# Optimization experiments

Hardware: AMD Instinct MI355X
Metric: run time of the kernel (lower is better)

## Reference

```python
import jax, jax.numpy as jnp
import numpy as np

MIN_C = 1e-5   # base_c * DYNAMIC_CURVATURE_MIN_RATIO
MAX_C = 10.0   # base_c * DYNAMIC_CURVATURE_MAX_RATIO
T = 0.7
EPS = 1e-7
B, IN_DIM, HID, OUT_DIM = 4096, 4096, 4096, 1024


def _artanh(x):
    x = jnp.clip(x, -1.0 + 1e-5, 1.0 - 1e-5)
    return 0.5 * jnp.log1p(2.0 * x / (1.0 - x))


def _mobius_scalar_mul(r, x, c):
    # r: python float, x: [B,D], c: [B,1] per-row curvature
    sqrt_c = jnp.sqrt(c)
    norm = jnp.clip(jnp.linalg.norm(x, axis=-1, keepdims=True), EPS)
    arg = jnp.clip(sqrt_c * norm, EPS, 1.0 - 1e-5)
    return jnp.tanh(r * _artanh(arg)) * x / (sqrt_c * norm)


def _mobius_add(x, y, c):
    xy = jnp.sum(x * y, axis=-1, keepdims=True)
    x2 = jnp.sum(x * x, axis=-1, keepdims=True)
    y2 = jnp.sum(y * y, axis=-1, keepdims=True)
    num = (1.0 + 2.0 * c * xy + c * y2) * x + (1.0 - c * x2) * y
    den = 1.0 + 2.0 * c * xy + c * c * x2 * y2
    return num / jnp.clip(den, EPS)


def poincare_ball_layer(h, u, c, t):
    # geodesic-style layer: ((1-t) (*) h) (+) (t (*) u) on the Poincare ball
    return _mobius_add(_mobius_scalar_mul(1.0 - t, h, c),
                       _mobius_scalar_mul(t, u, c), c)


def setup_inputs() -> dict:
    key = jax.random.key(0)
    ks = jax.random.split(key, 8)
    std = 0.02  # WEIGHT_INIT_STD_IMPROVED
    return {
        "x": jax.random.normal(ks[0], (B, IN_DIM), jnp.float32),
        "W1": jax.random.normal(ks[1], (IN_DIM, HID), jnp.float32) * std,
        "b1": jnp.zeros((HID,), jnp.float32),
        "W2": jax.random.normal(ks[2], (HID, HID), jnp.float32) * std,
        "b2": jnp.zeros((HID,), jnp.float32),
        "Wout": jax.random.normal(ks[3], (HID, OUT_DIM), jnp.float32) * std,
        "bout": jnp.zeros((OUT_DIM,), jnp.float32),
        "curv_feat": jax.random.normal(ks[4], (16,), jnp.float32) * 0.01,
        "curv_scale": jnp.ones((1,), jnp.float32) * 0.1,
        "proj": jax.random.normal(ks[5], (IN_DIM, 16), jnp.float32),
    }


def reference(x, W1, b1, W2, b2, Wout, bout, curv_feat, curv_scale, proj):
    x_flat = x.reshape(x.shape[0], -1)
    h = jnp.tanh(x_flat @ W1 + b1)            # [B, HID]
    u = jax.nn.sigmoid(h @ W2 + b2)           # [B, HID]
    # adaptive curvature prediction (vectorized over batch)
    x_red = x_flat @ proj                     # [B, 16]
    feat_inter = x_red @ curv_feat            # [B]
    adj = jax.nn.sigmoid(feat_inter + curv_scale[0])
    c = MIN_C + (MAX_C - MIN_C) * adj         # [B]
    c = jnp.clip(c, MIN_C, MAX_C)[:, None]    # [B, 1]
    z = poincare_ball_layer(h, u, c, T)
    # NaN fallback per row (mirrors torch per-sample isnan check)
    z = jnp.where(jnp.any(jnp.isnan(z), axis=1, keepdims=True), h, z)
    return z @ Wout + bout
```

## Files before the change

kernel.cpp:

```cpp
#include <hip/hip_runtime.h>
#include <hip/hip_bf16.h>
#include <math.h>


typedef __attribute__((ext_vector_type(8))) __bf16 bf16x8;
typedef __attribute__((ext_vector_type(4))) float  f32x4;

constexpr int BATCH = 4096;
constexpr int IND   = 4096;
constexpr int HIDD  = 4096;
constexpr int OUTD  = 1024;
constexpr float T_C  = 0.7f;
constexpr float MINC = 1e-5f;
constexpr float MAXC = 10.0f;
constexpr float EPSV = 1e-7f;

__device__ __forceinline__ float bf2f(unsigned int us) {
    return __uint_as_float(us << 16);
}
__device__ __forceinline__ unsigned short f2bf(float f) {
    unsigned int u = __float_as_uint(f);
    u = (u + 0x7FFFu + ((u >> 16) & 1u)) >> 16;
    return (unsigned short)u;
}

__global__ __launch_bounds__(256)
void cast_curv(const float* __restrict__ x, const float* __restrict__ v,
               const float* __restrict__ cs,
               unsigned short* __restrict__ xb, float* __restrict__ c)
{
    const int row = blockIdx.x;
    const float* xr = x + (size_t)row * IND;
    unsigned short* ob = xb + (size_t)row * IND;
    float s = 0.f;
    for (int i = threadIdx.x; i < IND / 4; i += 256) {
        float4 w  = ((const float4*)xr)[i];
        float4 vv = ((const float4*)v)[i];
        s += w.x * vv.x + w.y * vv.y + w.z * vv.z + w.w * vv.w;
        ushort4 o;
        o.x = f2bf(w.x); o.y = f2bf(w.y); o.z = f2bf(w.z); o.w = f2bf(w.w);
        ((ushort4*)ob)[i] = o;
    }
    #pragma unroll
    for (int o = 32; o > 0; o >>= 1) s += __shfl_down(s, o, 64);
    __shared__ float red[4];
    if ((threadIdx.x & 63) == 0) red[threadIdx.x >> 6] = s;
    __syncthreads();
    if (threadIdx.x == 0) {
        float tot = red[0] + red[1] + red[2] + red[3];
        float adj = 1.0f / (1.0f + expf(-(tot + cs[0])));
        float cc  = MINC + (MAXC - MINC) * adj;
        c[row] = fminf(fmaxf(cc, MINC), MAXC);
    }
}

__global__ __launch_bounds__(256)
void transpose_cast(const float* __restrict__ in, unsigned short* __restrict__ out,
                    int K, int N)
{
    __shared__ float tile[32][33];
    const int k0 = blockIdx.y * 32;
    const int n0 = blockIdx.x * 32;
    const int t = threadIdx.x;
    #pragma unroll
    for (int i = 0; i < 4; i++) {
        int idx = t + i * 256;
        int r = idx >> 5, c = idx & 31;
        tile[r][c] = in[(size_t)(k0 + r) * N + n0 + c];
    }
    __syncthreads();
    #pragma unroll
    for (int i = 0; i < 4; i++) {
        int idx = t + i * 256;
        int r = idx >> 5, c = idx & 31;
        out[(size_t)(n0 + r) * K + k0 + c] = f2bf(tile[c][r]);
    }
}

template<int EPI>
__global__ __launch_bounds__(512)
void gemm256(const unsigned short* __restrict__ A,
             const unsigned short* __restrict__ Bt,
             const float* __restrict__ bias,
             unsigned short* __restrict__ outp,
             int N, int K)
{
    __shared__ unsigned short lds[4 * 256 * 64];
    unsigned short* Al = lds;
    unsigned short* Bl = lds + 2 * 256 * 64;

    const int t = threadIdx.x;
    const int w = t >> 6, l = t & 63;
    const int wr = w >> 2, wc = w & 3;
    const int lr = l & 15, lg = l >> 4;

    const int nwg = gridDim.x * gridDim.y;
    const int bid = blockIdx.y * gridDim.x + blockIdx.x;
    const int q8 = nwg >> 3, r8 = nwg & 7;
    const int xcd = bid & 7, off = bid >> 3;
    const int wgid = (xcd < r8 ? xcd * (q8 + 1) : r8 * (q8 + 1) + (xcd - r8) * q8) + off;
    const int by = wgid / gridDim.x;
    const int bx = wgid % gridDim.x;

    const int row0 = by * 256, col0 = bx * 256;
    const unsigned short* Ab = A  + (size_t)row0 * K;
    const unsigned short* Bb = Bt + (size_t)col0 * K;
    const int NT = K >> 6;

    f32x4 acc[8][4] = {};

    auto stage_half = [&](int kt, int buf, int mat, int h) {
        const int kb = kt * 128;
        const unsigned short* gb = mat ? Bb : Ab;
        unsigned short* lb = (mat ? Bl : Al) + buf * 16384 + h * 8192;
        #pragma unroll
        for (int qq = 0; qq < 2; qq++) {
            const int id  = qq * 512 + t;
            const int row = h * 128 + (id >> 3);
            const int cb  = (id & 7) * 16;
            const int scb = cb ^ ((row & 7) << 4);
            const char* src = (const char*)gb + (size_t)row * ((size_t)K * 2) + kb + scb;
            __builtin_amdgcn_global_load_lds(
                (const __attribute__((address_space(1))) unsigned int*)src,
                (__attribute__((address_space(3))) unsigned int*)(lb + id * 8), 16, 0, 0);
        }
    };

    stage_half(0, 0, 0, 0);
    stage_half(0, 0, 1, 0);
    stage_half(0, 0, 1, 1);
    stage_half(0, 0, 0, 1);
    asm volatile("s_waitcnt vmcnt(2)" ::: "memory");
    __builtin_amdgcn_s_barrier();

    const int sw = (lr & 7) << 4;
    const int c0 = (lg * 16) ^ sw;
    const int c1 = (64 + lg * 16) ^ sw;

    for (int kt = 0; kt < NT; ++kt) {
        const int buf = kt & 1, nb = buf ^ 1;
        const bool pre = (kt + 1 < NT);
        const char* AlB = (const char*)Al + buf * 32768 + (wr * 16 + lr) * 128;
        const char* BlB = (const char*)Bl + buf * 32768 + (wc * 64 + lr) * 128;

        bf16x8 bfk[4], afk[4];

        #pragma unroll
        for (int ni = 0; ni < 4; ni++) bfk[ni] = *(const bf16x8*)(BlB + ni * 2048 + c0);
        #pragma unroll
        for (int mi = 0; mi < 4; mi++) afk[mi] = *(const bf16x8*)(AlB + mi * 4096 + c0);
        if (pre) { stage_half(kt + 1, nb, 0, 0); stage_half(kt + 1, nb, 1, 0); }
        __builtin_amdgcn_s_setprio(1);
        #pragma unroll
        for (int mi = 0; mi < 4; mi++)
            #pragma unroll
            for (int ni = 0; ni < 4; ni++)
                acc[mi][ni] = __builtin_amdgcn_mfma_f32_16x16x32_bf16(
                    afk[mi], bfk[ni], acc[mi][ni], 0, 0, 0);
        __builtin_amdgcn_s_setprio(0);
        if (pre) asm volatile("s_waitcnt vmcnt(4)" ::: "memory");
        else     asm volatile("s_waitcnt vmcnt(0)" ::: "memory");
        __builtin_amdgcn_s_barrier();

        #pragma unroll
        for (int mi = 0; mi < 4; mi++) afk[mi] = *(const bf16x8*)(AlB + (4 + mi) * 4096 + c0);
        if (pre) { stage_half(kt + 1, nb, 1, 1); stage_half(kt + 1, nb, 0, 1); }
        __builtin_amdgcn_s_setprio(1);
        #pragma unroll
        for (int mi = 0; mi < 4; mi++)
            #pragma unroll
            for (int ni = 0; ni < 4; ni++)
                acc[4 + mi][ni] = __builtin_amdgcn_mfma_f32_16x16x32_bf16(
                    afk[mi], bfk[ni], acc[4 + mi][ni], 0, 0, 0);
        __builtin_amdgcn_s_setprio(0);
        __builtin_amdgcn_s_barrier();

        #pragma unroll
        for (int ni = 0; ni < 4; ni++) bfk[ni] = *(const bf16x8*)(BlB + ni * 2048 + c1);
        #pragma unroll
        for (int mi = 0; mi < 4; mi++) afk[mi] = *(const bf16x8*)(AlB + mi * 4096 + c1);
        __builtin_amdgcn_s_setprio(1);
        #pragma unroll
        for (int mi = 0; mi < 4; mi++)
            #pragma unroll
            for (int ni = 0; ni < 4; ni++)
                acc[mi][ni] = __builtin_amdgcn_mfma_f32_16x16x32_bf16(
                    afk[mi], bfk[ni], acc[mi][ni], 0, 0, 0);
        __builtin_amdgcn_s_setprio(0);
        __builtin_amdgcn_s_barrier();

        #pragma unroll
        for (int mi = 0; mi < 4; mi++) afk[mi] = *(const bf16x8*)(AlB + (4 + mi) * 4096 + c1);
        __builtin_amdgcn_s_setprio(1);
        #pragma unroll
        for (int mi = 0; mi < 4; mi++)
            #pragma unroll
            for (int ni = 0; ni < 4; ni++)
                acc[4 + mi][ni] = __builtin_amdgcn_mfma_f32_16x16x32_bf16(
                    afk[mi], bfk[ni], acc[4 + mi][ni], 0, 0, 0);
        __builtin_amdgcn_s_setprio(0);
        if (pre) asm volatile("s_waitcnt vmcnt(2)" ::: "memory");
        else     asm volatile("s_waitcnt vmcnt(0)" ::: "memory");
        __builtin_amdgcn_s_barrier();
    }

    const int colb = col0 + wc * 64;
    #pragma unroll
    for (int ni = 0; ni < 4; ni++) {
        const int cg = colb + ni * 16 + lr;
        const float bv = bias[cg];
        #pragma unroll
        for (int mi = 0; mi < 8; mi++) {
            #pragma unroll
            for (int r = 0; r < 4; r++) {
                const int rg = row0 + wr * 16 + mi * 32 + lg * 4 + r;
                float v = acc[mi][ni][r] + bv;
                if constexpr (EPI == 0) v = tanhf(v);
                else                    v = 1.0f / (1.0f + expf(-v));
                outp[(size_t)rg * N + cg] = f2bf(v);
            }
        }
    }
}

__global__ __launch_bounds__(256)
void gemm_bt_f32(const unsigned short* __restrict__ A,
                 const unsigned short* __restrict__ Bt,
                 const float* __restrict__ bias,
                 float* __restrict__ outp,
                 int N, int K)
{
    __shared__ unsigned short Asl[128 * 32];
    __shared__ unsigned short Bsl[128 * 32];

    const int t  = threadIdx.x;
    const int w  = t >> 6, l = t & 63;
    const int wr = w >> 1, wc = w & 1;
    const int row0 = blockIdx.y * 128;
    const int col0 = blockIdx.x * 128;

    const unsigned short* Ab = A  + (size_t)row0 * K;
    const unsigned short* Bb = Bt + (size_t)col0 * K;

    const int lr = l & 15;
    const int lk = (l >> 4) * 8;

    f32x4 acc[4][4] = {};

    for (int k0 = 0; k0 < K; k0 += 32) {
        __syncthreads();
        #pragma unroll
        for (int q = 0; q < 2; q++) {
            int idx = q * 256 + t;
            int r   = idx >> 2;
            int c8  = (idx & 3) * 8;
            __builtin_amdgcn_global_load_lds(
                (const __attribute__((address_space(1))) unsigned int*)(Ab + (size_t)r * K + k0 + c8),
                (__attribute__((address_space(3))) unsigned int*)(&Asl[idx * 8]), 16, 0, 0);
            __builtin_amdgcn_global_load_lds(
                (const __attribute__((address_space(1))) unsigned int*)(Bb + (size_t)r * K + k0 + c8),
                (__attribute__((address_space(3))) unsigned int*)(&Bsl[idx * 8]), 16, 0, 0);
        }
        __syncthreads();

        bf16x8 af[4], bfr[4];
        #pragma unroll
        for (int mi = 0; mi < 4; mi++)
            af[mi] = *(const bf16x8*)(&Asl[(wr * 64 + mi * 16 + lr) * 32 + lk]);
        #pragma unroll
        for (int ni = 0; ni < 4; ni++)
            bfr[ni] = *(const bf16x8*)(&Bsl[(wc * 64 + ni * 16 + lr) * 32 + lk]);

        #pragma unroll
        for (int mi = 0; mi < 4; mi++)
            #pragma unroll
            for (int ni = 0; ni < 4; ni++)
                acc[mi][ni] = __builtin_amdgcn_mfma_f32_16x16x32_bf16(
                    af[mi], bfr[ni], acc[mi][ni], 0, 0, 0);
    }

    const int colb = col0 + wc * 64;
    const int rowb = row0 + wr * 64 + (l >> 4) * 4;
    #pragma unroll
    for (int ni = 0; ni < 4; ni++) {
        const int cg = colb + ni * 16 + lr;
        const float bv = bias[cg];
        #pragma unroll
        for (int mi = 0; mi < 4; mi++)
            #pragma unroll
            for (int r = 0; r < 4; r++)
                outp[(size_t)(rowb + mi * 16 + r) * N + cg] = acc[mi][ni][r] + bv;
    }
}

__global__ __launch_bounds__(256)
void proj_cf(const float* __restrict__ proj, const float* __restrict__ cf,
             float* __restrict__ v)
{
    int i = blockIdx.x * 256 + threadIdx.x;
    if (i < IND) {
        float s = 0.f;
        #pragma unroll
        for (int j = 0; j < 16; j++) s += proj[i * 16 + j] * cf[j];
        v[i] = s;
    }
}

__global__ __launch_bounds__(256)
void poincare_kernel(const unsigned short* __restrict__ hb,
                     const unsigned short* __restrict__ ub,
                     const float* __restrict__ c,
                     unsigned short* __restrict__ zb)
{
    const int row = blockIdx.x;
    const int t = threadIdx.x;
    const size_t base = (size_t)row * HIDD;

    float hv[16], uv[16];
    float h2 = 0.f, u2 = 0.f, hu = 0.f;
    #pragma unroll
    for (int q = 0; q < 2; q++) {
        const int e0 = (q * 256 + t) * 8;
        uint4 hc = *(const uint4*)(hb + base + e0);
        uint4 uc = *(const uint4*)(ub + base + e0);
        const unsigned int hw[4] = {hc.x, hc.y, hc.z, hc.w};
        const unsigned int uw[4] = {uc.x, uc.y, uc.z, uc.w};
        #pragma unroll
        for (int i = 0; i < 4; i++) {
            float h0 = bf2f(hw[i] & 0xFFFFu), h1 = bf2f(hw[i] >> 16);
            float u0 = bf2f(uw[i] & 0xFFFFu), u1 = bf2f(uw[i] >> 16);
            hv[q * 8 + 2 * i]     = h0; hv[q * 8 + 2 * i + 1] = h1;
            uv[q * 8 + 2 * i]     = u0; uv[q * 8 + 2 * i + 1] = u1;
            h2 += h0 * h0 + h1 * h1;
            u2 += u0 * u0 + u1 * u1;
            hu += h0 * u0 + h1 * u1;
        }
    }
    #pragma unroll
    for (int o = 32; o > 0; o >>= 1) {
        h2 += __shfl_down(h2, o, 64);
        u2 += __shfl_down(u2, o, 64);
        hu += __shfl_down(hu, o, 64);
    }
    __shared__ float red[3][4];
    const int w = t >> 6;
    if ((t & 63) == 0) { red[0][w] = h2; red[1][w] = u2; red[2][w] = hu; }
    __syncthreads();
    h2 = red[0][0] + red[0][1] + red[0][2] + red[0][3];
    u2 = red[1][0] + red[1][1] + red[1][2] + red[1][3];
    hu = red[2][0] + red[2][1] + red[2][2] + red[2][3];

    const float cc = c[row];
    const float sc = sqrtf(cc);
    float nh = fmaxf(sqrtf(h2), EPSV);
    float nu = fmaxf(sqrtf(u2), EPSV);
    float ah = fminf(fmaxf(sc * nh, EPSV), 1.0f - 1e-5f);
    float au = fminf(fmaxf(sc * nu, EPSV), 1.0f - 1e-5f);
    float ath = 0.5f * log1pf(2.0f * ah / (1.0f - ah));
    float atu = 0.5f * log1pf(2.0f * au / (1.0f - au));
    float alpha = tanhf((1.0f - T_C) * ath) / (sc * nh);
    float beta  = tanhf(T_C * atu) / (sc * nu);
    float x2 = alpha * alpha * h2;
    float y2 = beta * beta * u2;
    float xy = alpha * beta * hu;
    float den = 1.0f + 2.0f * cc * xy + cc * cc * x2 * y2;
    den = fmaxf(den, EPSV);
    float ca = (1.0f + 2.0f * cc * xy + cc * y2) * alpha / den;
    float cb = (1.0f - cc * x2) * beta / den;
    if (isnan(ca) || isnan(cb)) { ca = 1.0f; cb = 0.0f; }

    #pragma unroll
    for (int q = 0; q < 2; q++) {
        const int e0 = (q * 256 + t) * 8;
        unsigned int ow[4];
        #pragma unroll
        for (int i = 0; i < 4; i++) {
            float z0 = ca * hv[q * 8 + 2 * i]     + cb * uv[q * 8 + 2 * i];
            float z1 = ca * hv[q * 8 + 2 * i + 1] + cb * uv[q * 8 + 2 * i + 1];
            ow[i] = (unsigned int)f2bf(z0) | ((unsigned int)f2bf(z1) << 16);
        }
        *(uint4*)(zb + base + e0) = make_uint4(ow[0], ow[1], ow[2], ow[3]);
    }
}

extern "C" void kernel_launch(void* const* d_in, const int* in_sizes, int n_in,
                              void* d_out, int out_size, void* d_ws, size_t ws_size,
                              hipStream_t stream)
{
    const float* x    = (const float*)d_in[0];
    const float* W1   = (const float*)d_in[1];
    const float* b1   = (const float*)d_in[2];
    const float* W2   = (const float*)d_in[3];
    const float* b2   = (const float*)d_in[4];
    const float* Wout = (const float*)d_in[5];
    const float* bout = (const float*)d_in[6];
    const float* cf   = (const float*)d_in[7];
    const float* cs   = (const float*)d_in[8];
    const float* proj = (const float*)d_in[9];
    float* out = (float*)d_out;

    char* ws = (char*)d_ws;
    unsigned short* x_bf = (unsigned short*)(ws);
    unsigned short* w_bf = (unsigned short*)(ws + (33554432));
    unsigned short* h_bf = (unsigned short*)(ws + (67108864));
    unsigned short* u_bf = (unsigned short*)(ws + (100663296));
    float* vvec = (float*)(ws + 134217728);
    float* cvec = (float*)(ws + 134217728 + 16384);

    proj_cf<<<IND / 256, 256, 0, stream>>>(proj, cf, vvec);
    cast_curv<<<BATCH, 256, 0, stream>>>(x, vvec, cs, x_bf, cvec);

    transpose_cast<<<dim3(HIDD / 32, IND / 32), 256, 0, stream>>>(W1, w_bf, IND, HIDD);
    gemm256<0><<<dim3(HIDD / 256, BATCH / 256), 512, 0, stream>>>(x_bf, w_bf, b1, h_bf, HIDD, IND);

    transpose_cast<<<dim3(HIDD / 32, HIDD / 32), 256, 0, stream>>>(W2, w_bf, HIDD, HIDD);
    gemm256<1><<<dim3(HIDD / 256, BATCH / 256), 512, 0, stream>>>(h_bf, w_bf, b2, u_bf, HIDD, HIDD);

    poincare_kernel<<<BATCH, 256, 0, stream>>>(h_bf, u_bf, cvec, x_bf);

    transpose_cast<<<dim3(OUTD / 32, HIDD / 32), 256, 0, stream>>>(Wout, w_bf, HIDD, OUTD);
    gemm_bt_f32<<<dim3(OUTD / 128, BATCH / 128), 256, 0, stream>>>(x_bf, w_bf, bout, out, OUTD, HIDD);
}
```

Measured before the change: 434.9 us.

## Software-pipeline LDS fragment reads across MFMA phases in gemm256

Restructures the GEMM main loop so LDS fragment loads for the next phase, including the first phase of the next k-tile, are issued before the current MFMA block runs. Separate register sets are used per phase instead of one reused set. Global-to-LDS staging is regrouped, and a full vmcnt(0) wait is added at the end of each iteration. Launch bounds now request 2 blocks per CU, which caps registers while register pressure from the extra fragment buffers goes up, so spilling is a risk.

```diff
diff --git a/kernel.cpp b/kernel.cpp
--- a/kernel.cpp
+++ b/kernel.cpp
@@ -78,7 +78,7 @@
 }
 
 template<int EPI>
-__global__ __launch_bounds__(512)
+__global__ __launch_bounds__(512, 2)
 void gemm256(const unsigned short* __restrict__ A,
              const unsigned short* __restrict__ Bt,
              const float* __restrict__ bias,
@@ -126,6 +126,12 @@
         }
     };
 
+    const int sw = (lr & 7) << 4;
+    const int c0 = (lg * 16) ^ sw;
+    const int c1 = (64 + lg * 16) ^ sw;
+    const int aoff = (wr * 16 + lr) * 128;
+    const int boff = (wc * 64 + lr) * 128;
+
     stage_half(0, 0, 0, 0);
     stage_half(0, 0, 1, 0);
     stage_half(0, 0, 1, 1);
@@ -133,74 +139,87 @@
     asm volatile("s_waitcnt vmcnt(2)" ::: "memory");
     __builtin_amdgcn_s_barrier();
 
-    const int sw = (lr & 7) << 4;
-    const int c0 = (lg * 16) ^ sw;
-    const int c1 = (64 + lg * 16) ^ sw;
+    bf16x8 bA[4], aA[4], aB[4], bB[4], aC[4], aD[4];
+    {
+        const char* AlB = (const char*)Al + aoff;
+        const char* BlB = (const char*)Bl + boff;
+        #pragma unroll
+        for (int ni = 0; ni < 4; ni++) bA[ni] = *(const bf16x8*)(BlB + ni * 2048 + c0);
+        #pragma unroll
+        for (int mi = 0; mi < 4; mi++) aA[mi] = *(const bf16x8*)(AlB + mi * 4096 + c0);
+    }
+    asm volatile("s_waitcnt vmcnt(0)" ::: "memory");
+    __builtin_amdgcn_s_barrier();
 
     for (int kt = 0; kt < NT; ++kt) {
         const int buf = kt & 1, nb = buf ^ 1;
         const bool pre = (kt + 1 < NT);
-        const char* AlB = (const char*)Al + buf * 32768 + (wr * 16 + lr) * 128;
-        const char* BlB = (const char*)Bl + buf * 32768 + (wc * 64 + lr) * 128;
-
-        bf16x8 bfk[4], afk[4];
-
-        #pragma unroll
-        for (int ni = 0; ni < 4; ni++) bfk[ni] = *(const bf16x8*)(BlB + ni * 2048 + c0);
-        #pragma unroll
-        for (int mi = 0; mi < 4; mi++) afk[mi] = *(const bf16x8*)(AlB + mi * 4096 + c0);
-        if (pre) { stage_half(kt + 1, nb, 0, 0); stage_half(kt + 1, nb, 1, 0); }
+        const char* AlB = (const char*)Al + buf * 32768 + aoff;
+        const char* BlB = (const char*)Bl + buf * 32768 + boff;
+
+        #pragma unroll
+        for (int mi = 0; mi < 4; mi++) aB[mi] = *(const bf16x8*)(AlB + (4 + mi) * 4096 + c0);
+        if (pre) {
+            stage_half(kt + 1, nb, 0, 0);
+            stage_half(kt + 1, nb, 1, 0);
+            stage_half(kt + 1, nb, 1, 1);
+        }
         __builtin_amdgcn_s_setprio(1);
         #pragma unroll
         for (int mi = 0; mi < 4; mi++)
             #pragma unroll
             for (int ni = 0; ni < 4; ni++)
                 acc[mi][ni] = __builtin_amdgcn_mfma_f32_16x16x32_bf16(
-                    afk[mi], bfk[ni], acc[mi][ni], 0, 0, 0);
+                    aA[mi], bA[ni], acc[mi][ni], 0, 0, 0);
         __builtin_amdgcn_s_setprio(0);
-        if (pre) asm volatile("s_waitcnt vmcnt(4)" ::: "memory");
-        else     asm volatile("s_waitcnt vmcnt(0)" ::: "memory");
         __builtin_amdgcn_s_barrier();
 
         #pragma unroll
-        for (int mi = 0; mi < 4; mi++) afk[mi] = *(const bf16x8*)(AlB + (4 + mi) * 4096 + c0);
-        if (pre) { stage_half(kt + 1, nb, 1, 1); stage_half(kt + 1, nb, 0, 1); }
+        for (int ni = 0; ni < 4; ni++) bB[ni] = *(const bf16x8*)(BlB + ni * 2048 + c1);
+        #pragma unroll
+        for (int mi = 0; mi < 4; mi++) aC[mi] = *(const bf16x8*)(AlB + mi * 4096 + c1);
+        if (pre) stage_half(kt + 1, nb, 0, 1);
         __builtin_amdgcn_s_setprio(1);
         #pragma unroll
         for (int mi = 0; mi < 4; mi++)
             #pragma unroll
             for (int ni = 0; ni < 4; ni++)
                 acc[4 + mi][ni] = __builtin_amdgcn_mfma_f32_16x16x32_bf16(
-                    afk[mi], bfk[ni], acc[4 + mi][ni], 0, 0, 0);
+                    aB[mi], bA[ni], acc[4 + mi][ni], 0, 0, 0);
         __builtin_amdgcn_s_setprio(0);
         __builtin_amdgcn_s_barrier();
 
         #pragma unroll
-        for (int ni = 0; ni < 4; ni++) bfk[ni] = *(const bf16x8*)(BlB + ni * 2048 + c1);
-        #pragma unroll
-        for (int mi = 0; mi < 4; mi++) afk[mi] = *(const bf16x8*)(AlB + mi * 4096 + c1);
+        for (int mi = 0; mi < 4; mi++) aD[mi] = *(const bf16x8*)(AlB + (4 + mi) * 4096 + c1);
         __builtin_amdgcn_s_setprio(1);
         #pragma unroll
         for (int mi = 0; mi < 4; mi++)
             #pragma unroll
             for (int ni = 0; ni < 4; ni++)
                 acc[mi][ni] = __builtin_amdgcn_mfma_f32_16x16x32_bf16(
-                    afk[mi], bfk[ni], acc[mi][ni], 0, 0, 0);
-        __builtin_amdgcn_s_setprio(0);
-        __builtin_amdgcn_s_barrier();
-
-        #pragma unroll
-        for (int mi = 0; mi < 4; mi++) afk[mi] = *(const bf16x8*)(AlB + (4 + mi) * 4096 + c1);
-        __builtin_amdgcn_s_setprio(1);
-        #pragma unroll
-        for (int mi = 0; mi < 4; mi++)
-            #pragma unroll
-            for (int ni = 0; ni < 4; ni++)
-                acc[4 + mi][ni] = __builtin_amdgcn_mfma_f32_16x16x32_bf16(
-                    afk[mi], bfk[ni], acc[4 + mi][ni], 0, 0, 0);
+                    aC[mi], bB[ni], acc[mi][ni], 0, 0, 0);
         __builtin_amdgcn_s_setprio(0);
         if (pre) asm volatile("s_waitcnt vmcnt(2)" ::: "memory");
         else     asm volatile("s_waitcnt vmcnt(0)" ::: "memory");
+        __builtin_amdgcn_s_barrier();
+
+        if (pre) {
+            const char* nAlB = (const char*)Al + nb * 32768 + aoff;
+            const char* nBlB = (const char*)Bl + nb * 32768 + boff;
+            #pragma unroll
+            for (int ni = 0; ni < 4; ni++) bA[ni] = *(const bf16x8*)(nBlB + ni * 2048 + c0);
+            #pragma unroll
+            for (int mi = 0; mi < 4; mi++) aA[mi] = *(const bf16x8*)(nAlB + mi * 4096 + c0);
+        }
+        __builtin_amdgcn_s_setprio(1);
+        #pragma unroll
+        for (int mi = 0; mi < 4; mi++)
+            #pragma unroll
+            for (int ni = 0; ni < 4; ni++)
+                acc[4 + mi][ni] = __builtin_amdgcn_mfma_f32_16x16x32_bf16(
+                    aD[mi], bB[ni], acc[4 + mi][ni], 0, 0, 0);
+        __builtin_amdgcn_s_setprio(0);
+        asm volatile("s_waitcnt vmcnt(0)" ::: "memory");
         __builtin_amdgcn_s_barrier();
     }
 
```

After: 436.5 us. Within noise of the previous version (+0.4%).
